# Kernel optimization log

Measured on AMD Instinct MI355X. Metric: run time of the kernel, lower is better.

Reference implementation:

```python
import jax, jax.numpy as jnp
import numpy as np

B, C, D, H, W = 2, 4, 64, 96, 96
INF = 1e10  # stand-in for +inf in fp32 EDT init


def _edt_pass(f, axis):
    # one separable pass of squared EDT along `axis`:
    # d[i] = min_j f[j] + (i - j)^2  (brute-force lower envelope)
    f = jnp.moveaxis(f, axis, -1)
    n = f.shape[-1]
    i = jnp.arange(n)
    ij2 = ((i[:, None] - i[None, :]) ** 2).astype(f.dtype)  # [n, n]
    d = jnp.min(f[..., None, :] + ij2, axis=-1)  # [..., n]
    return jnp.moveaxis(d, -1, axis)


def edt(bg):
    # Euclidean distance transform matching scipy.distance_transform_edt:
    # for nonzero voxels of `bg`, distance to nearest zero voxel.
    f = jnp.where(bg != 0, jnp.asarray(INF, bg.dtype), jnp.asarray(0.0, bg.dtype))
    for ax in range(bg.ndim):  # scipy is called on the full [B,D,H,W] array
        f = _edt_pass(f, ax)
    return jnp.sqrt(f)


def setup_inputs() -> dict:
    key = jax.random.key(0)
    k1, k2 = jax.random.split(key)
    logits = jax.random.normal(k1, (B, C, D, H, W), jnp.float32)
    targets = jax.random.randint(k2, (B, D, H, W), 0, C, dtype=jnp.int32)
    return {"logits": logits, "targets": targets}


def reference(logits, targets):
    probs = jax.nn.sigmoid(logits)                       # [B,C,D,H,W]
    nc = probs.shape[1]
    one_hot = jax.nn.one_hot(targets, nc, dtype=probs.dtype)  # [B,D,H,W,C]
    binary = one_hot.sum(-1)                             # [B,D,H,W] (== 1 for valid targets)
    dist = edt(1.0 - binary)                             # [B,D,H,W]
    # loss = mean over classes of sum(prob_c * dist) / numel(prob_c)
    per_class = jnp.sum(probs * dist[:, None], axis=(0, 2, 3, 4)) / dist.size
    return jnp.sum(per_class) / nc
```

## Files before the change

kernel.cpp:

```cpp
#include <hip/hip_runtime.h>


#define EDT_INF 1e10f

constexpr int Bb = 2, Cc = 4, Dd = 64, Hh = 96, Ww = 96;
constexpr int HW  = Hh * Ww;
constexpr int DHW = Dd * HW;
constexpr int N4  = Bb * DHW;
constexpr int NI4 = N4 / 4;
constexpr int KF_BLOCKS = 288;

__device__ __forceinline__ float evalB(const int* __restrict__ t, int b, int q) {
    int tv = t[b * DHW + q];
    float fb = (tv >= 0 && tv < Cc) ? 0.0f : EDT_INF;
    if (fb == 0.0f) return 0.0f;
    int to = t[(1 - b) * DHW + q];
    float fo = (to >= 0 && to < Cc) ? 0.0f : EDT_INF;
    return fminf(fb, fo + 1.0f);
}

__device__ float evalD(const int* __restrict__ t, int b, int d, int hw) {
    float best = evalB(t, b, d * HW + hw);
    for (int r = 1; r < Dd; ++r) {
        float r2 = (float)(r * r);
        if (r2 >= best) break;
        int jm = d - r, jp = d + r;
        if (jm >= 0) best = fminf(best, evalB(t, b, jm * HW + hw) + r2);
        if (jp < Dd) best = fminf(best, evalB(t, b, jp * HW + hw) + r2);
    }
    return best;
}

__device__ float evalH(const int* __restrict__ t, int b, int d, int h, int w) {
    float best = evalD(t, b, d, h * Ww + w);
    for (int r = 1; r < Hh; ++r) {
        float r2 = (float)(r * r);
        if (r2 >= best) break;
        int jm = h - r, jp = h + r;
        if (jm >= 0) best = fminf(best, evalD(t, b, d, jm * Ww + w) + r2);
        if (jp < Hh) best = fminf(best, evalD(t, b, d, jp * Ww + w) + r2);
    }
    return best;
}

__device__ float evalW(const int* __restrict__ t, int b, int d, int h, int w) {
    float best = evalH(t, b, d, h, w);
    for (int r = 1; r < Ww; ++r) {
        float r2 = (float)(r * r);
        if (r2 >= best) break;
        int jm = w - r, jp = w + r;
        if (jm >= 0) best = fminf(best, evalH(t, b, d, h, jm) + r2);
        if (jp < Ww) best = fminf(best, evalH(t, b, d, h, jp) + r2);
    }
    return best;
}

__global__ __launch_bounds__(256) void kf_all(const int* __restrict__ targets,
                                              const float* __restrict__ logits,
                                              float* __restrict__ out) {
    float acc = 0.0f;
    for (int i4 = blockIdx.x * 256 + threadIdx.x; i4 < NI4;
         i4 += KF_BLOCKS * 256) {
        const int e = i4 * 4;
        const int4 t4 = *reinterpret_cast<const int4*>(&targets[e]);
        const bool fast = (t4.x >= 0 && t4.x < Cc) && (t4.y >= 0 && t4.y < Cc) &&
                          (t4.z >= 0 && t4.z < Cc) && (t4.w >= 0 && t4.w < Cc);
        if (!fast) {
            int b   = e / DHW;
            int rem = e - b * DHW;
            int d   = rem / HW;
            int r2_ = rem - d * HW;
            int h   = r2_ / Ww;
            int w0  = r2_ - h * Ww;
            for (int l = 0; l < 4; ++l) {
                float dist = sqrtf(evalW(targets, b, d, h, w0 + l));
                if (dist != 0.0f) {
                    const float* lp = logits + (size_t)b * Cc * DHW + rem + l;
                    #pragma unroll
                    for (int c = 0; c < Cc; ++c) {
                        float x = lp[(size_t)c * DHW];
                        acc += dist * __builtin_amdgcn_rcpf(1.0f + __expf(-x));
                    }
                }
            }
        }
    }

    #pragma unroll
    for (int off = 32; off > 0; off >>= 1) acc += __shfl_down(acc, off, 64);
    __shared__ float sw[4];
    const int lane = threadIdx.x & 63, wid = threadIdx.x >> 6;
    if (lane == 0) sw[wid] = acc;
    __syncthreads();
    if (threadIdx.x == 0) {
        float total = ((sw[0] + sw[1]) + sw[2]) + sw[3];
        atomicAdd(out, total * (1.0f / ((float)N4 * (float)Cc)));
    }
}

extern "C" void kernel_launch(void* const* d_in, const int* in_sizes, int n_in,
                              void* d_out, int out_size, void* d_ws, size_t ws_size,
                              hipStream_t stream) {
    const float* logits  = (const float*)d_in[0];
    const int*   targets = (const int*)d_in[1];
    float* out = (float*)d_out;

    hipMemsetAsync(out, 0, sizeof(float), stream);
    kf_all<<<dim3(KF_BLOCKS), dim3(256), 0, stream>>>(targets, logits, out);
}
```

Baseline: 15.28 us.

## Replace memset and atomic reduction with cooperative grid-sync final reduction

The separate memset launch and per-block atomicAdd are replaced by a single cooperative kernel launch. Each block writes its partial sum to workspace, the grid synchronises, and block 0 reduces the 288 partials and writes the output directly. The grid-stride loop also becomes a fixed unrolled loop of 4 int4 items per thread. The intent is to drop the extra memset launch and the atomic traffic, at the cost of a grid-wide barrier and cooperative-launch overhead.

```diff
diff --git a/kernel.cpp b/kernel.cpp
--- a/kernel.cpp
+++ b/kernel.cpp
@@ -1,4 +1,7 @@
 #include <hip/hip_runtime.h>
+#include <hip/hip_cooperative_groups.h>
+
+namespace cg = cooperative_groups;
 
 
 #define EDT_INF 1e10f
@@ -8,7 +11,8 @@
 constexpr int DHW = Dd * HW;
 constexpr int N4  = Bb * DHW;
 constexpr int NI4 = N4 / 4;
-constexpr int KF_BLOCKS = 288;
+constexpr int NBLK = 288;
+constexpr int I4_PER_THREAD = 4;
 
 __device__ __forceinline__ float evalB(const int* __restrict__ t, int b, int q) {
     int tv = t[b * DHW + q];
@@ -55,12 +59,15 @@
     return best;
 }
 
-__global__ __launch_bounds__(256) void kf_all(const int* __restrict__ targets,
-                                              const float* __restrict__ logits,
-                                              float* __restrict__ out) {
+__global__ __launch_bounds__(256) void kf_coop(const int* __restrict__ targets,
+                                               const float* __restrict__ logits,
+                                               float* __restrict__ partials,
+                                               float* __restrict__ out) {
     float acc = 0.0f;
-    for (int i4 = blockIdx.x * 256 + threadIdx.x; i4 < NI4;
-         i4 += KF_BLOCKS * 256) {
+    const int base = blockIdx.x * (256 * I4_PER_THREAD);
+    #pragma unroll
+    for (int k = 0; k < I4_PER_THREAD; ++k) {
+        const int i4 = base + k * 256 + threadIdx.x;
         const int e = i4 * 4;
         const int4 t4 = *reinterpret_cast<const int4*>(&targets[e]);
         const bool fast = (t4.x >= 0 && t4.x < Cc) && (t4.y >= 0 && t4.y < Cc) &&
@@ -92,19 +99,34 @@
     const int lane = threadIdx.x & 63, wid = threadIdx.x >> 6;
     if (lane == 0) sw[wid] = acc;
     __syncthreads();
-    if (threadIdx.x == 0) {
-        float total = ((sw[0] + sw[1]) + sw[2]) + sw[3];
-        atomicAdd(out, total * (1.0f / ((float)N4 * (float)Cc)));
+    if (threadIdx.x == 0)
+        partials[blockIdx.x] = ((sw[0] + sw[1]) + sw[2]) + sw[3];
+
+    cg::this_grid().sync();
+
+    if (blockIdx.x == 0) {
+        float a2 = partials[threadIdx.x];
+        if ((int)threadIdx.x < NBLK - 256) a2 += partials[256 + threadIdx.x];
+        #pragma unroll
+        for (int off = 32; off > 0; off >>= 1) a2 += __shfl_down(a2, off, 64);
+        __shared__ float sw2[4];
+        if (lane == 0) sw2[wid] = a2;
+        __syncthreads();
+        if (threadIdx.x == 0)
+            out[0] = (((sw2[0] + sw2[1]) + sw2[2]) + sw2[3]) *
+                     (1.0f / ((float)N4 * (float)Cc));
     }
 }
 
 extern "C" void kernel_launch(void* const* d_in, const int* in_sizes, int n_in,
                               void* d_out, int out_size, void* d_ws, size_t ws_size,
                               hipStream_t stream) {
+    const int*   targets = (const int*)d_in[1];
     const float* logits  = (const float*)d_in[0];
-    const int*   targets = (const int*)d_in[1];
     float* out = (float*)d_out;
+    float* partials = (float*)d_ws;
 
-    hipMemsetAsync(out, 0, sizeof(float), stream);
-    kf_all<<<dim3(KF_BLOCKS), dim3(256), 0, stream>>>(targets, logits, out);
+    void* args[] = {(void*)&targets, (void*)&logits, (void*)&partials, (void*)&out};
+    hipLaunchCooperativeKernel((const void*)kf_coop, dim3(NBLK), dim3(256),
+                               args, 0, stream);
 }
```

Result: slower. 44.77 us (+192.9%).
